# Kernel tuning notes

Hardware: AMD Instinct MI355X
Metric: run time of the kernel (lower is better)

The kernel has to match this reference:

```python
import jax, jax.numpy as jnp
import numpy as np

B, T, D = 2, 2048, 2048
H, KVH = 16, 4
HD = D // H            # 128
HALF = HD // 2         # 64
EPS = 1e-6


def zc_rmsnorm(x, scale):
    # zero-centred RMSNorm: (1+scale) * x / rms(x), rms in fp32
    rms = jnp.sqrt(jnp.mean(x.astype(jnp.float32) ** 2, axis=-1, keepdims=True) + EPS)
    return ((1.0 + scale) * x / rms).astype(x.dtype)


def apply_rope(x, cos, sin):
    # x: [B, h, T, HD]; cos/sin: [T, HALF]
    t = x.shape[2]
    c = cos[:t][None, None, :, :]
    s = sin[:t][None, None, :, :]
    x1, x2 = x[..., :HALF], x[..., HALF:]
    return jnp.concatenate([x1 * c - x2 * s, x2 * c + x1 * s], axis=-1)


def setup_inputs() -> dict:
    key = jax.random.key(0)
    ks = jax.random.split(key, 8)
    std = 0.02
    res_std = 0.02 / np.sqrt(2 * 24)
    q_input = jax.random.normal(ks[0], (B, T, D), jnp.float32)
    kv_input = jax.random.normal(ks[1], (B, T, D), jnp.float32)
    mask = jnp.tril(jnp.ones((T, T), bool))[None, None, :, :]
    inv_freq = 1.0 / (10000.0 ** (jnp.arange(0, HALF, dtype=jnp.float32) / HALF))
    ang = jnp.arange(T, dtype=jnp.float32)[:, None] * inv_freq[None, :]
    cos, sin = jnp.cos(ang), jnp.sin(ang)
    Wq = jax.random.normal(ks[2], (D, D), jnp.float32) * std
    Wk = jax.random.normal(ks[3], (D, KVH * HD), jnp.float32) * std
    Wv = jax.random.normal(ks[4], (D, KVH * HD), jnp.float32) * std
    q_scale = jnp.zeros((HD,), jnp.float32)
    k_scale = jnp.zeros((HD,), jnp.float32)
    Wo = jax.random.normal(ks[5], (D, D), jnp.float32) * res_std
    return {"q_input": q_input, "kv_input": kv_input, "mask": mask,
            "cos": cos, "sin": sin, "Wq": Wq, "Wk": Wk, "Wv": Wv,
            "q_scale": q_scale, "k_scale": k_scale, "Wo": Wo}


def reference(q_input, kv_input, mask, cos, sin, Wq, Wk, Wv, q_scale, k_scale, Wo):
    b = q_input.shape[0]
    q = (q_input @ Wq).reshape(b, -1, H, HD).transpose(0, 2, 1, 3)      # [B,H,T,HD]
    k = (kv_input @ Wk).reshape(b, -1, KVH, HD).transpose(0, 2, 1, 3)   # [B,KVH,T,HD]
    v = (kv_input @ Wv).reshape(b, -1, KVH, HD).transpose(0, 2, 1, 3)
    q = zc_rmsnorm(q, q_scale)
    k = zc_rmsnorm(k, k_scale)
    rep = H // KVH
    k = jnp.repeat(k, rep, axis=1)
    v = jnp.repeat(v, rep, axis=1)
    q = apply_rope(q, cos, sin)
    k = apply_rope(k, cos, sin)
    scale = jnp.sqrt(jnp.float32(HD))
    scores = jnp.einsum('bhqd,bhkd->bhqk', q, k) / scale                # [B,H,T,T]
    scores = jnp.where(mask, scores, jnp.finfo(scores.dtype).min)
    attn = jax.nn.softmax(scores, axis=-1)
    out = jnp.einsum('bhqk,bhkd->bhqd', attn, v)
    out = out.transpose(0, 2, 1, 3).reshape(b, -1, D)
    return out @ Wo
```

## Files before the change

### kernel.cpp

```cpp
#include <hip/hip_runtime.h>

#define NB 2
#define NT 2048
#define ND 2048
#define NH 16
#define NKVH 4
#define NHD 128
#define NHALF 64
#define NREP (NH / NKVH)
#define MFIX 12.0f

typedef __bf16 bf16x8 __attribute__((ext_vector_type(8)));
typedef unsigned short u16x8 __attribute__((ext_vector_type(8)));
typedef unsigned short u16x4 __attribute__((ext_vector_type(4)));
typedef float f32x4 __attribute__((ext_vector_type(4)));

__device__ __forceinline__ unsigned short f2b(float f) {
  union { float f; unsigned int u; } v; v.f = f;
  unsigned int r = v.u + 0x7FFFu + ((v.u >> 16) & 1u);
  return (unsigned short)(r >> 16);
}

__device__ __forceinline__ void glds16(const unsigned short* g, unsigned short* l) {
  __builtin_amdgcn_global_load_lds(
      (__attribute__((address_space(1))) unsigned int*)(unsigned long long)g,
      (__attribute__((address_space(3))) unsigned int*)(unsigned int)(unsigned long long)l,
      16, 0, 0);
}

__device__ __forceinline__ void f2bf_body(const float* __restrict__ in,
                                          unsigned short* __restrict__ out, int lb) {
  const size_t i = (size_t)(lb * 256 + threadIdx.x) * 8;
  float4 a = *(const float4*)(in + i);
  float4 b = *(const float4*)(in + i + 4);
  u16x8 r;
  r[0] = f2b(a.x); r[1] = f2b(a.y); r[2] = f2b(a.z); r[3] = f2b(a.w);
  r[4] = f2b(b.x); r[5] = f2b(b.y); r[6] = f2b(b.z); r[7] = f2b(b.w);
  *(u16x8*)(out + i) = r;
}

__device__ __forceinline__ void wtrans_body(const float* __restrict__ in,
                                            unsigned short* __restrict__ out,
                                            int K, int N, int bx, int by,
                                            float (*tile)[33]) {
  const int k0 = by * 32, n0 = bx * 32;
  const int x = threadIdx.x & 31, y8 = threadIdx.x >> 5;
#pragma unroll
  for (int j = 0; j < 4; ++j) {
    const int y = y8 + j * 8;
    tile[y][x] = in[(size_t)(k0 + y) * N + n0 + x];
  }
  __syncthreads();
#pragma unroll
  for (int j = 0; j < 4; ++j) {
    const int y = y8 + j * 8;
    out[(size_t)(n0 + y) * K + k0 + x] = f2b(tile[x][y]);
  }
}

__global__ __launch_bounds__(256) void prep_all(const float* __restrict__ q_input,
                                                unsigned short* __restrict__ Qb16,
                                                const float* __restrict__ kv_input,
                                                unsigned short* __restrict__ KVb16,
                                                const float* __restrict__ Wq,
                                                unsigned short* __restrict__ Wqt,
                                                const float* __restrict__ Wk,
                                                const float* __restrict__ Wv,
                                                unsigned short* __restrict__ WkvT,
                                                const float* __restrict__ Wo,
                                                unsigned short* __restrict__ Wot) {
  __shared__ float tile[32][33];
  const int l = blockIdx.x;
  if (l < 4096) {
    f2bf_body(q_input, Qb16, l);
  } else if (l < 8192) {
    f2bf_body(kv_input, KVb16, l - 4096);
  } else if (l < 12288) {
    const int l2 = l - 8192;
    wtrans_body(Wq, Wqt, 2048, 2048, l2 & 63, l2 >> 6, tile);
  } else if (l < 13312) {
    const int l2 = l - 12288;
    wtrans_body(Wk, WkvT, 2048, 512, l2 & 15, l2 >> 4, tile);
  } else if (l < 14336) {
    const int l2 = l - 13312;
    wtrans_body(Wv, WkvT + (size_t)512 * 2048, 2048, 512, l2 & 15, l2 >> 4, tile);
  } else {
    const int l2 = l - 14336;
    wtrans_body(Wo, Wot, 2048, 2048, l2 & 63, l2 >> 6, tile);
  }
}

__device__ __forceinline__ void gemm_mm(const unsigned short* __restrict__ A,
                                        const unsigned short* __restrict__ Bt,
                                        int K, int m0, int n0,
                                        unsigned short* As, unsigned short* Bs,
                                        f32x4 (&acc)[4][4]) {
  const int tid = threadIdx.x;
  const int wave = tid >> 6, lane = tid & 63;
  const int wm = wave >> 1, wn = wave & 1;
  const int quad = lane >> 4, c = lane & 15;
  const int lr = lane >> 3;
  const int gsw = ((lane & 7) ^ lr) * 8;

  const unsigned short* pa[4];
  const unsigned short* pb[4];
  unsigned short* da[4];
  unsigned short* db[4];
#pragma unroll
  for (int j = 0; j < 4; ++j) {
    const int rb = j * 32 + wave * 8;
    pa[j] = A + (size_t)(m0 + rb + lr) * K + gsw;
    pb[j] = Bt + (size_t)(n0 + rb + lr) * K + gsw;
    da[j] = As + rb * 64;
    db[j] = Bs + rb * 64;
  }

  const f32x4 zero = {0.f, 0.f, 0.f, 0.f};
#pragma unroll
  for (int sm = 0; sm < 4; ++sm)
#pragma unroll
    for (int sn = 0; sn < 4; ++sn) acc[sm][sn] = zero;

  const int nsteps = K >> 6;
  int cur = 0;

#pragma unroll
  for (int j = 0; j < 4; ++j) { glds16(pa[j], da[j]); glds16(pb[j], db[j]); }
  __syncthreads();

  for (int t = 0; t < nsteps; ++t) {
    const int nxt = (cur ^ 1) * (128 * 64);
    if (t + 1 < nsteps) {
      const int kn = (t + 1) << 6;
#pragma unroll
      for (int j = 0; j < 4; ++j) {
        glds16(pa[j] + kn, da[j] + nxt);
        glds16(pb[j] + kn, db[j] + nxt);
      }
    }
    const unsigned short* Ab = As + cur * (128 * 64);
    const unsigned short* Bb = Bs + cur * (128 * 64);
#pragma unroll
    for (int kk = 0; kk < 2; ++kk) {
      const int g = ((kk * 4 + quad) ^ (c & 7)) * 8;
      bf16x8 af[4];
#pragma unroll
      for (int sm = 0; sm < 4; ++sm)
        af[sm] = *(const bf16x8*)&Ab[(wm * 64 + sm * 16 + c) * 64 + g];
#pragma unroll
      for (int sn = 0; sn < 4; ++sn) {
        bf16x8 bfr = *(const bf16x8*)&Bb[(wn * 64 + sn * 16 + c) * 64 + g];
#pragma unroll
        for (int sm = 0; sm < 4; ++sm)
          acc[sm][sn] = __builtin_amdgcn_mfma_f32_16x16x32_bf16(af[sm], bfr, acc[sm][sn], 0, 0, 0);
      }
    }
    __syncthreads();
    cur ^= 1;
  }
}

__global__ __launch_bounds__(256) void gemm128(const unsigned short* __restrict__ A,
                                               const unsigned short* __restrict__ Bt,
                                               float* __restrict__ C,
                                               int M, int N, int K) {
  __shared__ __align__(16) unsigned char smem[65536];
  unsigned short* As = (unsigned short*)smem;
  unsigned short* Bs = (unsigned short*)(smem + 32768);
  const int gx = gridDim.x;
  const int nwg = gx * gridDim.y;
  int lin = blockIdx.y * gx + blockIdx.x;
  lin = (lin & 7) * (nwg >> 3) + (lin >> 3);
  const int m0 = (lin / gx) * 128, n0 = (lin % gx) * 128;
  f32x4 acc[4][4];
  gemm_mm(A, Bt, K, m0, n0, As, Bs, acc);
  const int tid = threadIdx.x;
  const int wave = tid >> 6, lane = tid & 63;
  const int wm = wave >> 1, wn = wave & 1;
  const int quad = lane >> 4, c = lane & 15;
#pragma unroll
  for (int sm = 0; sm < 4; ++sm)
#pragma unroll
    for (int sn = 0; sn < 4; ++sn) {
      const int row = m0 + wm * 64 + sm * 16 + quad * 4;
      const int col = n0 + wn * 64 + sn * 16 + c;
#pragma unroll
      for (int r = 0; r < 4; ++r)
        C[(size_t)(row + r) * N + col] = acc[sm][sn][r];
    }
}

__device__ __forceinline__ void epi_normrope(f32x4 (&acc)[4][4], float* xb,
                                             unsigned short* __restrict__ dst,
                                             const float* __restrict__ scale,
                                             const float* __restrict__ cosp,
                                             const float* __restrict__ sinp,
                                             int t0, float outscale) {
  const int tid = threadIdx.x;
  const int wave = tid >> 6, lane = tid & 63;
  const int wm = wave >> 1, wn = wave & 1;
  const int quad = lane >> 4, c = lane & 15;
#pragma unroll
  for (int sm = 0; sm < 4; ++sm)
#pragma unroll
    for (int sn = 0; sn < 4; ++sn) {
      const int row = wm * 64 + sm * 16 + quad * 4;
      const int col = wn * 64 + sn * 16 + c;
#pragma unroll
      for (int r = 0; r < 4; ++r)
        xb[(row + r) * 128 + col] = acc[sm][sn][r];
    }
  __syncthreads();
#pragma unroll
  for (int sm = 0; sm < 4; ++sm) {
#pragma unroll
    for (int r = 0; r < 4; ++r) {
      const int row = wm * 64 + sm * 16 + quad * 4 + r;
      float par[4];
      float ps = 0.f;
#pragma unroll
      for (int sn = 0; sn < 4; ++sn) {
        const float own = acc[sm][sn][r];
        par[sn] = xb[row * 128 + ((wn ^ 1) * 64 + sn * 16 + c)];
        ps += own * own + par[sn] * par[sn];
      }
      ps += __shfl_xor(ps, 1, 64);
      ps += __shfl_xor(ps, 2, 64);
      ps += __shfl_xor(ps, 4, 64);
      ps += __shfl_xor(ps, 8, 64);
      const float inv = 1.0f / sqrtf(ps * (1.0f / NHD) + 1e-6f);
      const int t = t0 + row;
#pragma unroll
      for (int sn = 0; sn < 4; ++sn) {
        const int d = wn * 64 + sn * 16 + c;
        const int dd = sn * 16 + c;
        const float n_own = (1.0f + scale[d]) * acc[sm][sn][r] * inv;
        const float n_par = (1.0f + scale[d ^ 64]) * par[sn] * inv;
        const float cc = cosp[t * NHALF + dd], ss = sinp[t * NHALF + dd];
        const float o = (wn == 0) ? (n_own * cc - n_par * ss)
                                  : (n_own * cc + n_par * ss);
        dst[(size_t)row * NHD + d] = f2b(o * outscale);
      }
    }
  }
}

__device__ __forceinline__ void epi_vtrans(f32x4 (&acc)[4][4],
                                           unsigned short* vb,
                                           unsigned short* __restrict__ dst) {
  const int tid = threadIdx.x;
  const int wave = tid >> 6, lane = tid & 63;
  const int wm = wave >> 1, wn = wave & 1;
  const int quad = lane >> 4, c = lane & 15;
#pragma unroll
  for (int sm = 0; sm < 4; ++sm)
#pragma unroll
    for (int sn = 0; sn < 4; ++sn) {
      const int row = wm * 64 + sm * 16 + quad * 4;
      const int col = wn * 64 + sn * 16 + c;
      u16x4 pk;
      pk[0] = f2b(acc[sm][sn][0]); pk[1] = f2b(acc[sm][sn][1]);
      pk[2] = f2b(acc[sm][sn][2]); pk[3] = f2b(acc[sm][sn][3]);
      *(u16x4*)&vb[col * 136 + row] = pk;
    }
  __syncthreads();
#pragma unroll
  for (int i = 0; i < 32; ++i) {
    const int d = wave * 32 + i;
    const unsigned int v = *(const unsigned int*)&vb[d * 136 + lane * 2];
    *(unsigned int*)&dst[(size_t)d * NT + lane * 2] = v;
  }
}

__global__ __launch_bounds__(256) void gemm_qkv(const unsigned short* __restrict__ Aq,
                                                const unsigned short* __restrict__ Wqt,
                                                const unsigned short* __restrict__ Akv,
                                                const unsigned short* __restrict__ Wkv,
                                                unsigned short* __restrict__ Qh,
                                                unsigned short* __restrict__ Kh,
                                                unsigned short* __restrict__ Vtg,
                                                const float* __restrict__ q_scale,
                                                const float* __restrict__ k_scale,
                                                const float* __restrict__ cosp,
                                                const float* __restrict__ sinp) {
  __shared__ __align__(16) unsigned char smem[65536];
  unsigned short* As = (unsigned short*)smem;
  unsigned short* Bs = (unsigned short*)(smem + 32768);
  int lin = blockIdx.x;
  lin = (lin & 7) * 96 + (lin >> 3);
  f32x4 acc[4][4];
  if (lin < 512) {
    const int m0 = (lin >> 4) * 128, n0 = (lin & 15) * 128;
    gemm_mm(Aq, Wqt, 2048, m0, n0, As, Bs, acc);
    const int b = m0 >> 11, t0 = m0 & 2047, h = n0 >> 7;
    epi_normrope(acc, (float*)smem,
                 Qh + ((size_t)(b * NH + h) * NT + t0) * NHD,
                 q_scale, cosp, sinp, t0, 0.08838834764831845f);
  } else {
    const int l2 = lin - 512;
    const int m0 = (l2 >> 3) * 128, n0 = (l2 & 7) * 128;
    gemm_mm(Akv, Wkv, 2048, m0, n0, As, Bs, acc);
    const int b = m0 >> 11, t0 = m0 & 2047;
    if (n0 < 512) {
      const int g = n0 >> 7;
      epi_normrope(acc, (float*)smem,
                   Kh + ((size_t)(b * NKVH + g) * NT + t0) * NHD,
                   k_scale, cosp, sinp, t0, 1.0f);
    } else {
      const int g = (n0 - 512) >> 7;
      epi_vtrans(acc, (unsigned short*)smem,
                 Vtg + ((size_t)(b * NKVH + g) * NHD) * NT + t0);
    }
  }
}

__global__ __launch_bounds__(256, 3) void attn64(const unsigned short* __restrict__ Qh,
                                                 const unsigned short* __restrict__ Kh,
                                                 const unsigned short* __restrict__ Vtg,
                                                 unsigned short* __restrict__ O) {
  __shared__ unsigned short Kt[64 * 132];
  __shared__ unsigned short Vt[128 * 68];
  __shared__ unsigned short Pt[64 * 68];
  const int bh = blockIdx.x;
  const int b = bh / NH, h = bh % NH, g = h / NREP;
  const int y = blockIdx.y;
  const int a = y & 7, bb = y >> 3;
  const int qt = (bb == 0) ? a : (bb == 1) ? a + 8 : (bb == 2) ? 31 - a : 23 - a;
  const int tid = threadIdx.x;
  const int w = tid >> 6, lane = tid & 63;
  const int quad = lane >> 4, c = lane & 15;

  bf16x8 qf[4];
  {
    const unsigned short* qp =
        Qh + ((size_t)(b * NH + h) * NT + qt * 64 + w * 16 + c) * NHD + quad * 8;
#pragma unroll
    for (int ch = 0; ch < 4; ++ch) qf[ch] = *(const bf16x8*)(qp + ch * 32);
  }

  f32x4 acc_o[8] = {};
  float lsum[4] = {0.f, 0.f, 0.f, 0.f};
  const size_t kbase = (size_t)(b * NKVH + g) * NT * NHD;
  const size_t vbase = (size_t)(b * NKVH + g) * NHD * NT;
  const int nkt = qt + 1;

  u16x8 kreg[4], vreg[4];
#pragma unroll
  for (int j = 0; j < 4; ++j) {
    const int f = j * 256 + tid;
    kreg[j] = *(const u16x8*)&Kh[kbase + (size_t)(f >> 4) * NHD + (f & 15) * 8];
    vreg[j] = *(const u16x8*)&Vtg[vbase + (size_t)(f >> 3) * NT + (f & 7) * 8];
  }

  for (int kt = 0; kt < nkt; ++kt) {
#pragma unroll
    for (int j = 0; j < 4; ++j) {
      const int f = j * 256 + tid;
      *(u16x8*)&Kt[(f >> 4) * 132 + (f & 15) * 8] = kreg[j];
      *(u16x8*)&Vt[(f >> 3) * 68 + (f & 7) * 8] = vreg[j];
    }
    __syncthreads();

    if (kt + 1 < nkt) {
      const int k0 = (kt + 1) * 64;
#pragma unroll
      for (int j = 0; j < 4; ++j) {
        const int f = j * 256 + tid;
        kreg[j] = *(const u16x8*)&Kh[kbase + (size_t)(k0 + (f >> 4)) * NHD + (f & 15) * 8];
        vreg[j] = *(const u16x8*)&Vtg[vbase + (size_t)(f >> 3) * NT + k0 + (f & 7) * 8];
      }
    }

    f32x4 s[4] = {};
#pragma unroll
    for (int n = 0; n < 4; ++n)
#pragma unroll
      for (int ch = 0; ch < 4; ++ch) {
        bf16x8 kf = *(const bf16x8*)&Kt[(n * 16 + c) * 132 + ch * 32 + quad * 8];
        s[n] = __builtin_amdgcn_mfma_f32_16x16x32_bf16(qf[ch], kf, s[n], 0, 0, 0);
      }

    const bool dmask = (kt == qt);
#pragma unroll
    for (int r = 0; r < 4; ++r) {
      float v0 = s[0][r], v1 = s[1][r], v2 = s[2][r], v3 = s[3][r];
      const int lrow = w * 16 + quad * 4 + r;
      if (dmask) {
        if (c > lrow) v0 = -1e30f;
        if (16 + c > lrow) v1 = -1e30f;
        if (32 + c > lrow) v2 = -1e30f;
        if (48 + c > lrow) v3 = -1e30f;
      }
      const float p0 = __expf(v0 - MFIX), p1 = __expf(v1 - MFIX);
      const float p2 = __expf(v2 - MFIX), p3 = __expf(v3 - MFIX);
      lsum[r] += (p0 + p1) + (p2 + p3);
      Pt[lrow * 68 + c] = f2b(p0);
      Pt[lrow * 68 + 16 + c] = f2b(p1);
      Pt[lrow * 68 + 32 + c] = f2b(p2);
      Pt[lrow * 68 + 48 + c] = f2b(p3);
    }

#pragma unroll
    for (int kc2 = 0; kc2 < 2; ++kc2) {
      bf16x8 pf = *(const bf16x8*)&Pt[(w * 16 + c) * 68 + kc2 * 32 + quad * 8];
#pragma unroll
      for (int n2 = 0; n2 < 8; ++n2) {
        bf16x8 vf = *(const bf16x8*)&Vt[(n2 * 16 + c) * 68 + kc2 * 32 + quad * 8];
        acc_o[n2] = __builtin_amdgcn_mfma_f32_16x16x32_bf16(pf, vf, acc_o[n2], 0, 0, 0);
      }
    }
    __syncthreads();
  }

#pragma unroll
  for (int r = 0; r < 4; ++r) {
    float l = lsum[r];
    l += __shfl_xor(l, 1, 64);
    l += __shfl_xor(l, 2, 64);
    l += __shfl_xor(l, 4, 64);
    l += __shfl_xor(l, 8, 64);
    lsum[r] = l;
  }

#pragma unroll
  for (int r = 0; r < 4; ++r) {
    const float invl = 1.0f / lsum[r];
    const int qrow = qt * 64 + w * 16 + quad * 4 + r;
    unsigned short* op = O + ((size_t)(b * NT + qrow) * NH + h) * NHD + c;
#pragma unroll
    for (int n2 = 0; n2 < 8; ++n2) op[n2 * 16] = f2b(acc_o[n2][r] * invl);
  }
}

extern "C" void kernel_launch(void* const* d_in, const int* in_sizes, int n_in,
                              void* d_out, int out_size, void* d_ws, size_t ws_size,
                              hipStream_t stream) {
  (void)in_sizes; (void)n_in; (void)out_size; (void)ws_size;
  const float* q_input  = (const float*)d_in[0];
  const float* kv_input = (const float*)d_in[1];
  const float* cosp = (const float*)d_in[3];
  const float* sinp = (const float*)d_in[4];
  const float* Wq = (const float*)d_in[5];
  const float* Wk = (const float*)d_in[6];
  const float* Wv = (const float*)d_in[7];
  const float* q_scale = (const float*)d_in[8];
  const float* k_scale = (const float*)d_in[9];
  const float* Wo = (const float*)d_in[10];
  float* out = (float*)d_out;

  char* p = (char*)d_ws;
  unsigned short* Qb16  = (unsigned short*)p; p += (size_t)NB * NT * ND * 2;
  unsigned short* KVb16 = (unsigned short*)p; p += (size_t)NB * NT * ND * 2;
  unsigned short* Qh  = (unsigned short*)p; p += (size_t)NB * NH * NT * NHD * 2;
  unsigned short* Kh  = (unsigned short*)p; p += (size_t)NB * NKVH * NT * NHD * 2;
  unsigned short* Vtg = (unsigned short*)p; p += (size_t)NB * NKVH * NT * NHD * 2;
  unsigned short* Wqt  = (unsigned short*)p; p += (size_t)ND * ND * 2;
  unsigned short* WkvT = (unsigned short*)p; p += (size_t)1024 * ND * 2;
  unsigned short* Wot  = (unsigned short*)p; p += (size_t)ND * ND * 2;
  unsigned short* Ob = Qb16;

  const dim3 blk(256);
  const int M = NB * NT;

  prep_all<<<dim3(18432), blk, 0, stream>>>(q_input, Qb16, kv_input, KVb16,
                                            Wq, Wqt, Wk, Wv, WkvT, Wo, Wot);

  gemm_qkv<<<dim3(768), blk, 0, stream>>>(Qb16, Wqt, KVb16, WkvT,
                                          Qh, Kh, Vtg, q_scale, k_scale, cosp, sinp);

  attn64<<<dim3(NB * NH, 32), blk, 0, stream>>>(Qh, Kh, Vtg, Ob);

  gemm128<<<dim3(ND / 128, M / 128), blk, 0, stream>>>(Ob, Wot, out, M, ND, ND);
}
```

Before: 346.8 us.

## Single-buffer QKV GEMM LDS and split epilogues to halve shared memory

The fused QKV projection kernel now uses a single-buffered K loop with 32 KB of LDS instead of a double-buffered 64 KB layout. The RMSNorm+RoPE and V-transpose epilogues are split into two passes so they fit in the smaller scratch space. The aim is to fit more workgroups per CU so their memory latency overlaps, at the cost of losing in-block prefetch overlap and adding extra barriers. The bf16 conversion also switches to the native __bf16 cast instead of manual rounding.

```diff
diff --git a/kernel.cpp b/kernel.cpp
--- a/kernel.cpp
+++ b/kernel.cpp
@@ -16,9 +16,9 @@
 typedef float f32x4 __attribute__((ext_vector_type(4)));
 
 __device__ __forceinline__ unsigned short f2b(float f) {
-  union { float f; unsigned int u; } v; v.f = f;
-  unsigned int r = v.u + 0x7FFFu + ((v.u >> 16) & 1u);
-  return (unsigned short)(r >> 16);
+  union { __bf16 h; unsigned short u; } v;
+  v.h = (__bf16)f;
+  return v.u;
 }
 
 __device__ __forceinline__ void glds16(const unsigned short* g, unsigned short* l) {
@@ -90,11 +90,12 @@
   }
 }
 
-__device__ __forceinline__ void gemm_mm(const unsigned short* __restrict__ A,
-                                        const unsigned short* __restrict__ Bt,
-                                        int K, int m0, int n0,
-                                        unsigned short* As, unsigned short* Bs,
-                                        f32x4 (&acc)[4][4]) {
+
+__device__ __forceinline__ void gemm_mm_db(const unsigned short* __restrict__ A,
+                                           const unsigned short* __restrict__ Bt,
+                                           int K, int m0, int n0,
+                                           unsigned short* As, unsigned short* Bs,
+                                           f32x4 (&acc)[4][4]) {
   const int tid = threadIdx.x;
   const int wave = tid >> 6, lane = tid & 63;
   const int wm = wave >> 1, wn = wave & 1;
@@ -123,7 +124,6 @@
 
   const int nsteps = K >> 6;
   int cur = 0;
-
 #pragma unroll
   for (int j = 0; j < 4; ++j) { glds16(pa[j], da[j]); glds16(pb[j], db[j]); }
   __syncthreads();
@@ -157,6 +157,65 @@
     }
     __syncthreads();
     cur ^= 1;
+  }
+}
+
+__device__ __forceinline__ void gemm_mm_sb(const unsigned short* __restrict__ A,
+                                           const unsigned short* __restrict__ Bt,
+                                           int K, int m0, int n0,
+                                           unsigned short* As, unsigned short* Bs,
+                                           f32x4 (&acc)[4][4]) {
+  const int tid = threadIdx.x;
+  const int wave = tid >> 6, lane = tid & 63;
+  const int wm = wave >> 1, wn = wave & 1;
+  const int quad = lane >> 4, c = lane & 15;
+  const int lr = lane >> 3;
+  const int gsw = ((lane & 7) ^ lr) * 8;
+
+  const unsigned short* pa[4];
+  const unsigned short* pb[4];
+  unsigned short* da[4];
+  unsigned short* db[4];
+#pragma unroll
+  for (int j = 0; j < 4; ++j) {
+    const int rb = j * 32 + wave * 8;
+    pa[j] = A + (size_t)(m0 + rb + lr) * K + gsw;
+    pb[j] = Bt + (size_t)(n0 + rb + lr) * K + gsw;
+    da[j] = As + rb * 64;
+    db[j] = Bs + rb * 64;
+  }
+
+  const f32x4 zero = {0.f, 0.f, 0.f, 0.f};
+#pragma unroll
+  for (int sm = 0; sm < 4; ++sm)
+#pragma unroll
+    for (int sn = 0; sn < 4; ++sn) acc[sm][sn] = zero;
+
+  const int nsteps = K >> 6;
+  for (int t = 0; t < nsteps; ++t) {
+    const int kn = t << 6;
+#pragma unroll
+    for (int j = 0; j < 4; ++j) {
+      glds16(pa[j] + kn, da[j]);
+      glds16(pb[j] + kn, db[j]);
+    }
+    __syncthreads();
+#pragma unroll
+    for (int kk = 0; kk < 2; ++kk) {
+      const int g = ((kk * 4 + quad) ^ (c & 7)) * 8;
+      bf16x8 af[4];
+#pragma unroll
+      for (int sm = 0; sm < 4; ++sm)
+        af[sm] = *(const bf16x8*)&As[(wm * 64 + sm * 16 + c) * 64 + g];
+#pragma unroll
+      for (int sn = 0; sn < 4; ++sn) {
+        bf16x8 bfr = *(const bf16x8*)&Bs[(wn * 64 + sn * 16 + c) * 64 + g];
+#pragma unroll
+        for (int sm = 0; sm < 4; ++sm)
+          acc[sm][sn] = __builtin_amdgcn_mfma_f32_16x16x32_bf16(af[sm], bfr, acc[sm][sn], 0, 0, 0);
+      }
+    }
+    __syncthreads();
   }
 }
 
@@ -173,7 +232,7 @@
   lin = (lin & 7) * (nwg >> 3) + (lin >> 3);
   const int m0 = (lin / gx) * 128, n0 = (lin % gx) * 128;
   f32x4 acc[4][4];
-  gemm_mm(A, Bt, K, m0, n0, As, Bs, acc);
+  gemm_mm_db(A, Bt, K, m0, n0, As, Bs, acc);
   const int tid = threadIdx.x;
   const int wave = tid >> 6, lane = tid & 63;
   const int wm = wave >> 1, wn = wave & 1;
@@ -201,47 +260,55 @@
   const int wm = wave >> 1, wn = wave & 1;
   const int quad = lane >> 4, c = lane & 15;
 #pragma unroll
-  for (int sm = 0; sm < 4; ++sm)
-#pragma unroll
-    for (int sn = 0; sn < 4; ++sn) {
-      const int row = wm * 64 + sm * 16 + quad * 4;
-      const int col = wn * 64 + sn * 16 + c;
-#pragma unroll
-      for (int r = 0; r < 4; ++r)
-        xb[(row + r) * 128 + col] = acc[sm][sn][r];
-    }
-  __syncthreads();
-#pragma unroll
-  for (int sm = 0; sm < 4; ++sm) {
-#pragma unroll
-    for (int r = 0; r < 4; ++r) {
-      const int row = wm * 64 + sm * 16 + quad * 4 + r;
-      float par[4];
-      float ps = 0.f;
+  for (int p = 0; p < 2; ++p) {
+#pragma unroll
+    for (int ls = 0; ls < 2; ++ls) {
+      const int sm = 2 * p + ls;
+      const int lrow = wm * 32 + ls * 16 + quad * 4;
 #pragma unroll
       for (int sn = 0; sn < 4; ++sn) {
-        const float own = acc[sm][sn][r];
-        par[sn] = xb[row * 128 + ((wn ^ 1) * 64 + sn * 16 + c)];
-        ps += own * own + par[sn] * par[sn];
-      }
-      ps += __shfl_xor(ps, 1, 64);
-      ps += __shfl_xor(ps, 2, 64);
-      ps += __shfl_xor(ps, 4, 64);
-      ps += __shfl_xor(ps, 8, 64);
-      const float inv = 1.0f / sqrtf(ps * (1.0f / NHD) + 1e-6f);
-      const int t = t0 + row;
-#pragma unroll
-      for (int sn = 0; sn < 4; ++sn) {
-        const int d = wn * 64 + sn * 16 + c;
-        const int dd = sn * 16 + c;
-        const float n_own = (1.0f + scale[d]) * acc[sm][sn][r] * inv;
-        const float n_par = (1.0f + scale[d ^ 64]) * par[sn] * inv;
-        const float cc = cosp[t * NHALF + dd], ss = sinp[t * NHALF + dd];
-        const float o = (wn == 0) ? (n_own * cc - n_par * ss)
-                                  : (n_own * cc + n_par * ss);
-        dst[(size_t)row * NHD + d] = f2b(o * outscale);
-      }
-    }
+        const int col = wn * 64 + sn * 16 + c;
+#pragma unroll
+        for (int r = 0; r < 4; ++r)
+          xb[(lrow + r) * 128 + col] = acc[sm][sn][r];
+      }
+    }
+    __syncthreads();
+#pragma unroll
+    for (int ls = 0; ls < 2; ++ls) {
+      const int sm = 2 * p + ls;
+#pragma unroll
+      for (int r = 0; r < 4; ++r) {
+        const int lrow = wm * 32 + ls * 16 + quad * 4 + r;
+        const int row = wm * 64 + sm * 16 + quad * 4 + r;
+        float par[4];
+        float ps = 0.f;
+#pragma unroll
+        for (int sn = 0; sn < 4; ++sn) {
+          const float own = acc[sm][sn][r];
+          par[sn] = xb[lrow * 128 + ((wn ^ 1) * 64 + sn * 16 + c)];
+          ps += own * own + par[sn] * par[sn];
+        }
+        ps += __shfl_xor(ps, 1, 64);
+        ps += __shfl_xor(ps, 2, 64);
+        ps += __shfl_xor(ps, 4, 64);
+        ps += __shfl_xor(ps, 8, 64);
+        const float inv = 1.0f / sqrtf(ps * (1.0f / NHD) + 1e-6f);
+        const int t = t0 + row;
+#pragma unroll
+        for (int sn = 0; sn < 4; ++sn) {
+          const int d = wn * 64 + sn * 16 + c;
+          const int dd = sn * 16 + c;
+          const float n_own = (1.0f + scale[d]) * acc[sm][sn][r] * inv;
+          const float n_par = (1.0f + scale[d ^ 64]) * par[sn] * inv;
+          const float cc = cosp[t * NHALF + dd], ss = sinp[t * NHALF + dd];
+          const float o = (wn == 0) ? (n_own * cc - n_par * ss)
+                                    : (n_own * cc + n_par * ss);
+          dst[(size_t)row * NHD + d] = f2b(o * outscale);
+        }
+      }
+    }
+    __syncthreads();
   }
 }
 
@@ -253,22 +320,28 @@
   const int wm = wave >> 1, wn = wave & 1;
   const int quad = lane >> 4, c = lane & 15;
 #pragma unroll
-  for (int sm = 0; sm < 4; ++sm)
-#pragma unroll
-    for (int sn = 0; sn < 4; ++sn) {
-      const int row = wm * 64 + sm * 16 + quad * 4;
-      const int col = wn * 64 + sn * 16 + c;
-      u16x4 pk;
-      pk[0] = f2b(acc[sm][sn][0]); pk[1] = f2b(acc[sm][sn][1]);
-      pk[2] = f2b(acc[sm][sn][2]); pk[3] = f2b(acc[sm][sn][3]);
-      *(u16x4*)&vb[col * 136 + row] = pk;
-    }
-  __syncthreads();
-#pragma unroll
-  for (int i = 0; i < 32; ++i) {
-    const int d = wave * 32 + i;
-    const unsigned int v = *(const unsigned int*)&vb[d * 136 + lane * 2];
-    *(unsigned int*)&dst[(size_t)d * NT + lane * 2] = v;
+  for (int p = 0; p < 2; ++p) {
+#pragma unroll
+    for (int sm = 0; sm < 4; ++sm)
+#pragma unroll
+      for (int ls = 0; ls < 2; ++ls) {
+        const int sn = 2 * p + ls;
+        const int row = wm * 64 + sm * 16 + quad * 4;
+        const int lcol = wn * 32 + ls * 16 + c;
+        u16x4 pk;
+        pk[0] = f2b(acc[sm][sn][0]); pk[1] = f2b(acc[sm][sn][1]);
+        pk[2] = f2b(acc[sm][sn][2]); pk[3] = f2b(acc[sm][sn][3]);
+        *(u16x4*)&vb[lcol * 136 + row] = pk;
+      }
+    __syncthreads();
+#pragma unroll
+    for (int i = 0; i < 16; ++i) {
+      const int lcol = wave * 16 + i;
+      const int d = (lcol >> 5) * 64 + (2 * p + ((lcol >> 4) & 1)) * 16 + (lcol & 15);
+      const unsigned int v = *(const unsigned int*)&vb[lcol * 136 + lane * 2];
+      *(unsigned int*)&dst[(size_t)d * NT + lane * 2] = v;
+    }
+    __syncthreads();
   }
 }
 
@@ -283,15 +356,15 @@
                                                 const float* __restrict__ k_scale,
                                                 const float* __restrict__ cosp,
                                                 const float* __restrict__ sinp) {
-  __shared__ __align__(16) unsigned char smem[65536];
+  __shared__ __align__(16) unsigned char smem[32768];
   unsigned short* As = (unsigned short*)smem;
-  unsigned short* Bs = (unsigned short*)(smem + 32768);
+  unsigned short* Bs = (unsigned short*)(smem + 16384);
   int lin = blockIdx.x;
   lin = (lin & 7) * 96 + (lin >> 3);
   f32x4 acc[4][4];
   if (lin < 512) {
     const int m0 = (lin >> 4) * 128, n0 = (lin & 15) * 128;
-    gemm_mm(Aq, Wqt, 2048, m0, n0, As, Bs, acc);
+    gemm_mm_sb(Aq, Wqt, 2048, m0, n0, As, Bs, acc);
     const int b = m0 >> 11, t0 = m0 & 2047, h = n0 >> 7;
     epi_normrope(acc, (float*)smem,
                  Qh + ((size_t)(b * NH + h) * NT + t0) * NHD,
@@ -299,7 +372,7 @@
   } else {
     const int l2 = lin - 512;
     const int m0 = (l2 >> 3) * 128, n0 = (l2 & 7) * 128;
-    gemm_mm(Akv, Wkv, 2048, m0, n0, As, Bs, acc);
+    gemm_mm_sb(Akv, Wkv, 2048, m0, n0, As, Bs, acc);
     const int b = m0 >> 11, t0 = m0 & 2047;
     if (n0 < 512) {
       const int g = n0 >> 7;
```

New measurement: 361.1 us. +4.1%, slower.
